# Performance work log

Hardware: AMD Instinct MI355X
Metric: run time of the kernel (lower is better)

The kernel has to match this reference:

```python
import jax, jax.numpy as jnp
import numpy as np

B, S, E, H, DH = 4, 2048, 1024, 16, 64
W_STD = 0.02  # init scale so softmax logits stay in a sane range


def setup_inputs() -> dict:
    key = jax.random.key(0)
    kx, kq, kk, kv, ko = jax.random.split(key, 5)
    x = jax.random.normal(kx, (B, S, E), dtype=jnp.float32)
    # torch nn.Linear weight layout is [out_features, in_features]; stacked over heads -> [H, DH, E]
    Wq = jax.random.normal(kq, (H, DH, E), dtype=jnp.float32) * W_STD
    Wk = jax.random.normal(kk, (H, DH, E), dtype=jnp.float32) * W_STD
    Wv = jax.random.normal(kv, (H, DH, E), dtype=jnp.float32) * W_STD
    Wo = jax.random.normal(ko, (E, E), dtype=jnp.float32) * W_STD
    return {"x": x, "Wq": Wq, "Wk": Wk, "Wv": Wv, "Wo": Wo}


def reference(x, Wq, Wk, Wv, Wo):
    Bx, Sx, Ex = x.shape
    head_dim = Wq.shape[1]
    scale = head_dim ** 0.5
    # Batched per-head projections (equivalent to the per-head Linear loop): y = x @ W.T
    q = jnp.einsum('bse,hde->bhsd', x, Wq)  # [B,H,S,DH]
    k = jnp.einsum('bse,hde->bhsd', x, Wk)
    v = jnp.einsum('bse,hde->bhsd', x, Wv)
    scores = jnp.einsum('bhsd,bhtd->bhst', q, k) / scale  # [B,H,S,S]
    causal = jnp.tril(jnp.ones((Sx, Sx), dtype=bool))
    scores = jnp.where(causal, scores, -jnp.inf)
    weights = jax.nn.softmax(scores, axis=-1)
    attn = jnp.einsum('bhst,bhtd->bshd', weights, v)  # [B,S,H,DH]
    concat = attn.reshape(Bx, Sx, Ex)  # head concat along feature dim
    return concat @ Wo.T
```

## Files before the change

### kernel.cpp

```cpp
#include <hip/hip_runtime.h>
#include <cstdint>
#include <cstddef>

typedef __bf16 bf16_t;
typedef __bf16 bf16x8 __attribute__((ext_vector_type(8)));
typedef float f32x4 __attribute__((ext_vector_type(4)));

#define MFMA16(a, b, c) __builtin_amdgcn_mfma_f32_16x16x32_bf16((a), (b), (c), 0, 0, 0)

__global__ __launch_bounds__(256) void cvt_f32_bf16(const float* __restrict__ src,
                                                    bf16_t* __restrict__ dst, int n4) {
  int stride = gridDim.x * blockDim.x;
  for (int i = blockIdx.x * blockDim.x + threadIdx.x; i < n4; i += stride) {
    float4 v = *(const float4*)(src + (size_t)i * 4);
    ushort4 o;
    o.x = __builtin_bit_cast(unsigned short, (bf16_t)v.x);
    o.y = __builtin_bit_cast(unsigned short, (bf16_t)v.y);
    o.z = __builtin_bit_cast(unsigned short, (bf16_t)v.z);
    o.w = __builtin_bit_cast(unsigned short, (bf16_t)v.w);
    *(ushort4*)(dst + (size_t)i * 4) = o;
  }
}

__global__ __launch_bounds__(256) void cvt3_f32_bf16(const float* __restrict__ s0,
                                                     const float* __restrict__ s1,
                                                     const float* __restrict__ s2,
                                                     bf16_t* __restrict__ dst, int n4) {
  const float* src = (blockIdx.y == 0) ? s0 : (blockIdx.y == 1) ? s1 : s2;
  bf16_t* d = dst + (size_t)blockIdx.y * n4 * 4;
  int stride = gridDim.x * blockDim.x;
  for (int i = blockIdx.x * blockDim.x + threadIdx.x; i < n4; i += stride) {
    float4 v = *(const float4*)(src + (size_t)i * 4);
    ushort4 o;
    o.x = __builtin_bit_cast(unsigned short, (bf16_t)v.x);
    o.y = __builtin_bit_cast(unsigned short, (bf16_t)v.y);
    o.z = __builtin_bit_cast(unsigned short, (bf16_t)v.z);
    o.w = __builtin_bit_cast(unsigned short, (bf16_t)v.w);
    *(ushort4*)(d + (size_t)i * 4) = o;
  }
}

__device__ __forceinline__ void gload_lds16(const bf16_t* g, bf16_t* lds) {
  __builtin_amdgcn_global_load_lds(
      (const __attribute__((address_space(1))) unsigned int*)g,
      (__attribute__((address_space(3))) unsigned int*)lds, 16, 0, 0);
}

__device__ __forceinline__ bf16x8 lds_frag(const bf16_t* tile, int row, int g) {
  int byte = row * 128 + ((g ^ (row & 7)) << 4);
  return *(const bf16x8*)((const char*)tile + byte);
}

__device__ __forceinline__ unsigned cvt_pk_bf16(float lo, float hi) {
  unsigned r;
  asm("v_cvt_pk_bf16_f32 %0, %1, %2" : "=v"(r) : "v"(lo), "v"(hi));
  return r;
}

template <int EPI>
__global__ __launch_bounds__(256)
void gemm_bt(const bf16_t* __restrict__ A, const bf16_t* __restrict__ Bm,
             bf16_t* __restrict__ Qo, bf16_t* __restrict__ Ko,
             bf16_t* __restrict__ Vto, float* __restrict__ Co) {
  const int K = 1024;
  const int NX = (EPI == 0) ? 24 : 8;
  __shared__ bf16_t As[128 * 64];
  __shared__ bf16_t Bs[128 * 64];
  const int wave = threadIdx.x >> 6, lane = threadIdx.x & 63;
  const int lm = lane & 15, lg = lane >> 4;
  const int wm = wave >> 1, wn = wave & 1;

  const int cpx = gridDim.x >> 3;
  const int swz = (blockIdx.x & 7) * cpx + (blockIdx.x >> 3);
  const int tm = (swz / NX) * 128, tn = (swz % NX) * 128;

  f32x4 zero = {0.f, 0.f, 0.f, 0.f};
  f32x4 acc[4][4];
#pragma unroll
  for (int i = 0; i < 4; ++i)
#pragma unroll
    for (int j = 0; j < 4; ++j) acc[i][j] = zero;

  const int srow = lane >> 3;
  const int gs = lane & 7;

  for (int k0 = 0; k0 < K; k0 += 64) {
#pragma unroll
    for (int c = 0; c < 4; ++c) {
      int cc = wave * 4 + c;
      int row = cc * 8 + srow;
      int gsrc = gs ^ (row & 7);
      gload_lds16(A + (size_t)(tm + row) * K + k0 + gsrc * 8, &As[cc * 512]);
      gload_lds16(Bm + (size_t)(tn + row) * K + k0 + gsrc * 8, &Bs[cc * 512]);
    }
    __syncthreads();
#pragma unroll
    for (int kk = 0; kk < 2; ++kk) {
      bf16x8 af[4], bfr[4];
#pragma unroll
      for (int i = 0; i < 4; ++i) af[i] = lds_frag(As, wm * 64 + i * 16 + lm, kk * 4 + lg);
#pragma unroll
      for (int i = 0; i < 4; ++i) bfr[i] = lds_frag(Bs, wn * 64 + i * 16 + lm, kk * 4 + lg);
#pragma unroll
      for (int mi = 0; mi < 4; ++mi)
#pragma unroll
        for (int ni = 0; ni < 4; ++ni)
          acc[mi][ni] = MFMA16(af[mi], bfr[ni], acc[mi][ni]);
    }
    __syncthreads();
  }

#pragma unroll
  for (int mi = 0; mi < 4; ++mi) {
#pragma unroll
    for (int ni = 0; ni < 4; ++ni) {
      const int m0 = tm + wm * 64 + mi * 16 + lg * 4;
      const int n = tn + wn * 64 + ni * 16 + lm;
      if (EPI == 0) {
        int which = n >> 10, rem = n & 1023;
        int hh = rem >> 6, d = rem & 63;
        int bb = m0 >> 11, s0 = m0 & 2047;
        size_t bh = (size_t)bb * 16 + hh;
        if (which == 2) {
          uint2 pw;
          pw.x = cvt_pk_bf16(acc[mi][ni][0], acc[mi][ni][1]);
          pw.y = cvt_pk_bf16(acc[mi][ni][2], acc[mi][ni][3]);
          *(uint2*)(Vto + (bh * 64 + d) * 2048 + s0) = pw;
        } else {
#pragma unroll
          for (int r = 0; r < 4; ++r) {
            float v = acc[mi][ni][r];
            if (which == 0)
              Qo[(bh * 2048 + s0 + r) * 64 + d] = (bf16_t)(v * 0.18033688011112042f);
            else
              Ko[(bh * 2048 + s0 + r) * 64 + d] = (bf16_t)v;
          }
        }
      } else {
#pragma unroll
        for (int r = 0; r < 4; ++r) Co[(size_t)(m0 + r) * 1024 + n] = acc[mi][ni][r];
      }
    }
  }
}

__device__ __forceinline__ void sm_step(const f32x4& s0, const f32x4& s1,
                                        float& l_run, bf16_t* P, int gbase,
                                        bool diag, int lm, int lg, int qrel) {
  float tv[2][4];
#pragma unroll
  for (int nt = 0; nt < 2; ++nt)
#pragma unroll
    for (int r = 0; r < 4; ++r) {
      float v = nt ? s1[r] : s0[r];
      if (diag && (nt * 16 + lg * 4 + r > qrel)) v = -3.0e38f;
      tv[nt][r] = v;
    }
#pragma unroll
  for (int nt = 0; nt < 2; ++nt) {
    float p0 = __builtin_amdgcn_exp2f(tv[nt][0]);
    float p1 = __builtin_amdgcn_exp2f(tv[nt][1]);
    float p2 = __builtin_amdgcn_exp2f(tv[nt][2]);
    float p3 = __builtin_amdgcn_exp2f(tv[nt][3]);
    l_run += (p0 + p1) + (p2 + p3);
    uint2 pw;
    pw.x = cvt_pk_bf16(p0, p1);
    pw.y = cvt_pk_bf16(p2, p3);
    int gr = (gbase + nt * 2 + (lg >> 1)) ^ (lm & 7);
    *(uint2*)((char*)P + lm * 128 + gr * 16 + (lg & 1) * 8) = pw;
  }
}

__device__ __forceinline__ void pv_step(const bf16_t* P, int gbase, const bf16x8 bv[4],
                                        f32x4* acc, int lm, int lg) {
  int gr = (gbase + lg) ^ (lm & 7);
  bf16x8 pf = *(const bf16x8*)((const char*)P + lm * 128 + gr * 16);
#pragma unroll
  for (int nd = 0; nd < 4; ++nd) acc[nd] = MFMA16(bv[nd], pf, acc[nd]);
}

__global__ __launch_bounds__(256, 4)
void attn_fwd(const bf16_t* __restrict__ Q, const bf16_t* __restrict__ K,
              const bf16_t* __restrict__ Vt, bf16_t* __restrict__ Aout) {
  const int S = 2048;
  const int i = blockIdx.x;
  const int bh = (i & 7) * 8 + ((i >> 3) & 7);
  const int p = i >> 6;
  const int hL = p, hH = 31 - p;
  const int b = bh >> 4, h = bh & 15;
  const int w = threadIdx.x >> 6, lane = threadIdx.x & 63;
  const int lm = lane & 15, lg = lane >> 4;
  const int qrowL = hL * 64 + w * 16;
  const int qrowH = hH * 64 + w * 16;
  const int qrel = ((w & 1) << 4) + lm;

  const bf16_t* Qb = Q + (size_t)bh * S * 64;
  const bf16_t* Kb = K + (size_t)bh * S * 64;
  const bf16_t* Vb = Vt + (size_t)bh * 64 * S;

  __shared__ bf16_t Plds[4][1024];
  __shared__ bf16_t Ksb[2][4096];
  __shared__ bf16_t Vsb[2][4096];
  bf16_t* P = Plds[w];

  bf16x8 aqL[2], aqH[2];
#pragma unroll
  for (int kk = 0; kk < 2; ++kk) {
    aqL[kk] = *(const bf16x8*)(Qb + (size_t)(qrowL + lm) * 64 + kk * 32 + lg * 8);
    aqH[kk] = *(const bf16x8*)(Qb + (size_t)(qrowH + lm) * 64 + kk * 32 + lg * 8);
  }

  float lL = 0.f, lH = 0.f;
  f32x4 zero = {0.f, 0.f, 0.f, 0.f};
  f32x4 accL[4], accH[4];
#pragma unroll
  for (int nd = 0; nd < 4; ++nd) { accL[nd] = zero; accH[nd] = zero; }

  const int sLend = hL * 2 + (w >> 1);
  const int sHend = hH * 2 + (w >> 1);

  auto stage = [&](int buf, int t) {
    const int kv0 = t * 64;
#pragma unroll
    for (int j = 0; j < 2; ++j) {
      int c = w * 2 + j;
      int r = c * 8 + (lane >> 3);
      int gs = (lane & 7) ^ (r & 7);
      gload_lds16(Kb + (size_t)(kv0 + r) * 64 + gs * 8, Ksb[buf] + c * 512);
      gload_lds16(Vb + (size_t)r * S + kv0 + gs * 8, Vsb[buf] + c * 512);
    }
  };

  stage(0, 0);
  for (int t = 0; t <= hH; ++t) {
    if (t < hH) {
      stage((t + 1) & 1, t + 1);
      asm volatile("s_waitcnt vmcnt(4)" ::: "memory");
    } else {
      asm volatile("s_waitcnt vmcnt(0)" ::: "memory");
    }
    __builtin_amdgcn_s_barrier();
    asm volatile("" ::: "memory");
    const bf16_t* Ks_ = Ksb[t & 1];
    const bf16_t* Vs_ = Vsb[t & 1];
#pragma unroll
    for (int s32 = 0; s32 < 2; ++s32) {
      const int step = t * 2 + s32;
      const bool actH = step <= sHend;
      const bool actL = step <= sLend;
      if (actH) {
        bf16x8 kf[2][2], bv[4];
#pragma unroll
        for (int nt = 0; nt < 2; ++nt)
#pragma unroll
          for (int kk = 0; kk < 2; ++kk)
            kf[nt][kk] = lds_frag(Ks_, s32 * 32 + nt * 16 + lm, kk * 4 + lg);
#pragma unroll
        for (int nd = 0; nd < 4; ++nd)
          bv[nd] = lds_frag(Vs_, nd * 16 + lm, s32 * 4 + lg);
        f32x4 sh0 = MFMA16(kf[0][0], aqH[0], zero);
        sh0 = MFMA16(kf[0][1], aqH[1], sh0);
        f32x4 sh1 = MFMA16(kf[1][0], aqH[0], zero);
        sh1 = MFMA16(kf[1][1], aqH[1], sh1);
        f32x4 sl0, sl1;
        if (actL) {
          sl0 = MFMA16(kf[0][0], aqL[0], zero);
          sl0 = MFMA16(kf[0][1], aqL[1], sl0);
          sl1 = MFMA16(kf[1][0], aqL[0], zero);
          sl1 = MFMA16(kf[1][1], aqL[1], sl1);
        }
        sm_step(sh0, sh1, lH, P, 4, step == sHend, lm, lg, qrel);
        if (actL) sm_step(sl0, sl1, lL, P, 0, step == sLend, lm, lg, qrel);
        asm volatile("s_waitcnt lgkmcnt(0)" ::: "memory");
        pv_step(P, 4, bv, accH, lm, lg);
        if (actL) pv_step(P, 0, bv, accL, lm, lg);
      }
    }
    asm volatile("" ::: "memory");
    __builtin_amdgcn_s_barrier();
    asm volatile("" ::: "memory");
  }

  float lsH = lH, lsL = lL;
  lsH += __shfl_xor(lsH, 16); lsH += __shfl_xor(lsH, 32);
  lsL += __shfl_xor(lsL, 16); lsL += __shfl_xor(lsL, 32);
  const float rlH = 1.f / lsH, rlL = 1.f / lsL;
#pragma unroll
  for (int nd = 0; nd < 4; ++nd) {
    uint2 oH, oL;
    oH.x = cvt_pk_bf16(accH[nd][0] * rlH, accH[nd][1] * rlH);
    oH.y = cvt_pk_bf16(accH[nd][2] * rlH, accH[nd][3] * rlH);
    oL.x = cvt_pk_bf16(accL[nd][0] * rlL, accL[nd][1] * rlL);
    oL.y = cvt_pk_bf16(accL[nd][2] * rlL, accL[nd][3] * rlL);
    size_t col = (size_t)(h * 64 + nd * 16 + lg * 4);
    *(uint2*)(Aout + ((size_t)(b * 2048 + qrowH + lm)) * 1024 + col) = oH;
    *(uint2*)(Aout + ((size_t)(b * 2048 + qrowL + lm)) * 1024 + col) = oL;
  }
}

extern "C" void kernel_launch(void* const* d_in, const int* in_sizes, int n_in,
                              void* d_out, int out_size, void* d_ws, size_t ws_size,
                              hipStream_t stream) {
  (void)in_sizes; (void)n_in; (void)out_size; (void)ws_size;
  const float* x  = (const float*)d_in[0];
  const float* Wq = (const float*)d_in[1];
  const float* Wk = (const float*)d_in[2];
  const float* Wv = (const float*)d_in[3];
  const float* Wo = (const float*)d_in[4];

  char* w = (char*)d_ws;
  bf16_t* xb    = (bf16_t*)(w);
  bf16_t* wb    = (bf16_t*)(w + 16777216);
  bf16_t* wob   = (bf16_t*)(w + 23068672);
  bf16_t* qb    = (bf16_t*)(w + 25165824);
  bf16_t* kb    = (bf16_t*)(w + 41943040);
  bf16_t* vtb   = (bf16_t*)(w + 58720256);
  bf16_t* attnb = (bf16_t*)(w + 75497472);

  cvt_f32_bf16<<<512, 256, 0, stream>>>(x, xb, 8388608 / 4);
  cvt3_f32_bf16<<<dim3(128, 3), 256, 0, stream>>>(Wq, Wk, Wv, wb, 1048576 / 4);
  cvt_f32_bf16<<<256, 256, 0, stream>>>(Wo, wob, 1048576 / 4);

  gemm_bt<0><<<dim3(1536), 256, 0, stream>>>(xb, wb, qb, kb, vtb, nullptr);
  attn_fwd<<<dim3(1024), 256, 0, stream>>>(qb, kb, vtb, attnb);
  gemm_bt<1><<<dim3(512), 256, 0, stream>>>(attnb, wob, nullptr, nullptr, nullptr,
                                            (float*)d_out);
}
```

Baseline: 168.5 us.

## Merge conversion kernels and share K/V tiles across two query pairs per block

Folds the three f32-to-bf16 conversion launches into one kernel with a 2D grid, which removes launch overhead. The attention kernel now runs 512 threads as two groups of four waves. Each group handles a different low/high query-tile pair of the same head, so one staged K/V tile in LDS serves twice as many queries and the number of blocks is halved. The cost is that the block loops to the longer pair's end, which brings some load imbalance and idle steps for the shorter group. Larger blocks with more LDS may also lower occupancy.

After: 164.2 us. -2.5%, faster.

```diff
diff --git a/kernel.cpp b/kernel.cpp
--- a/kernel.cpp
+++ b/kernel.cpp
@@ -8,8 +8,25 @@
 
 #define MFMA16(a, b, c) __builtin_amdgcn_mfma_f32_16x16x32_bf16((a), (b), (c), 0, 0, 0)
 
-__global__ __launch_bounds__(256) void cvt_f32_bf16(const float* __restrict__ src,
-                                                    bf16_t* __restrict__ dst, int n4) {
+__global__ __launch_bounds__(256) void cvt_all(const float* __restrict__ x,
+                                               const float* __restrict__ Wq,
+                                               const float* __restrict__ Wk,
+                                               const float* __restrict__ Wv,
+                                               const float* __restrict__ Wo,
+                                               bf16_t* __restrict__ xb,
+                                               bf16_t* __restrict__ wb,
+                                               bf16_t* __restrict__ wob) {
+  const int y = blockIdx.y;
+  const float* src;
+  bf16_t* dst;
+  if (y < 8) {
+    src = x + (size_t)y * 1048576;
+    dst = xb + (size_t)y * 1048576;
+  } else if (y == 8)  { src = Wq; dst = wb; }
+  else if (y == 9)    { src = Wk; dst = wb + 1048576; }
+  else if (y == 10)   { src = Wv; dst = wb + 2097152; }
+  else                { src = Wo; dst = wob; }
+  const int n4 = 262144;
   int stride = gridDim.x * blockDim.x;
   for (int i = blockIdx.x * blockDim.x + threadIdx.x; i < n4; i += stride) {
     float4 v = *(const float4*)(src + (size_t)i * 4);
@@ -19,24 +36,6 @@
     o.z = __builtin_bit_cast(unsigned short, (bf16_t)v.z);
     o.w = __builtin_bit_cast(unsigned short, (bf16_t)v.w);
     *(ushort4*)(dst + (size_t)i * 4) = o;
-  }
-}
-
-__global__ __launch_bounds__(256) void cvt3_f32_bf16(const float* __restrict__ s0,
-                                                     const float* __restrict__ s1,
-                                                     const float* __restrict__ s2,
-                                                     bf16_t* __restrict__ dst, int n4) {
-  const float* src = (blockIdx.y == 0) ? s0 : (blockIdx.y == 1) ? s1 : s2;
-  bf16_t* d = dst + (size_t)blockIdx.y * n4 * 4;
-  int stride = gridDim.x * blockDim.x;
-  for (int i = blockIdx.x * blockDim.x + threadIdx.x; i < n4; i += stride) {
-    float4 v = *(const float4*)(src + (size_t)i * 4);
-    ushort4 o;
-    o.x = __builtin_bit_cast(unsigned short, (bf16_t)v.x);
-    o.y = __builtin_bit_cast(unsigned short, (bf16_t)v.y);
-    o.z = __builtin_bit_cast(unsigned short, (bf16_t)v.z);
-    o.w = __builtin_bit_cast(unsigned short, (bf16_t)v.w);
-    *(ushort4*)(d + (size_t)i * 4) = o;
   }
 }
 
@@ -179,26 +178,29 @@
   for (int nd = 0; nd < 4; ++nd) acc[nd] = MFMA16(bv[nd], pf, acc[nd]);
 }
 
-__global__ __launch_bounds__(256, 4)
+__global__ __launch_bounds__(512, 8)
 void attn_fwd(const bf16_t* __restrict__ Q, const bf16_t* __restrict__ K,
               const bf16_t* __restrict__ Vt, bf16_t* __restrict__ Aout) {
   const int S = 2048;
   const int i = blockIdx.x;
   const int bh = (i & 7) * 8 + ((i >> 3) & 7);
-  const int p = i >> 6;
-  const int hL = p, hH = 31 - p;
+  const int j = i >> 6;
   const int b = bh >> 4, h = bh & 15;
   const int w = threadIdx.x >> 6, lane = threadIdx.x & 63;
   const int lm = lane & 15, lg = lane >> 4;
-  const int qrowL = hL * 64 + w * 16;
-  const int qrowH = hH * 64 + w * 16;
-  const int qrel = ((w & 1) << 4) + lm;
+  const int g = w >> 2;
+  const int wg = w & 3;
+  const int p = j + 8 * g;
+  const int hL = p, hH = 31 - p;
+  const int qrowL = hL * 64 + wg * 16;
+  const int qrowH = hH * 64 + wg * 16;
+  const int qrel = ((wg & 1) << 4) + lm;
 
   const bf16_t* Qb = Q + (size_t)bh * S * 64;
   const bf16_t* Kb = K + (size_t)bh * S * 64;
   const bf16_t* Vb = Vt + (size_t)bh * 64 * S;
 
-  __shared__ bf16_t Plds[4][1024];
+  __shared__ bf16_t Plds[8][1024];
   __shared__ bf16_t Ksb[2][4096];
   __shared__ bf16_t Vsb[2][4096];
   bf16_t* P = Plds[w];
@@ -216,26 +218,24 @@
 #pragma unroll
   for (int nd = 0; nd < 4; ++nd) { accL[nd] = zero; accH[nd] = zero; }
 
-  const int sLend = hL * 2 + (w >> 1);
-  const int sHend = hH * 2 + (w >> 1);
+  const int sLend = hL * 2 + (wg >> 1);
+  const int sHend = hH * 2 + (wg >> 1);
+  const int tmax = 31 - j;
 
   auto stage = [&](int buf, int t) {
     const int kv0 = t * 64;
-#pragma unroll
-    for (int j = 0; j < 2; ++j) {
-      int c = w * 2 + j;
-      int r = c * 8 + (lane >> 3);
-      int gs = (lane & 7) ^ (r & 7);
-      gload_lds16(Kb + (size_t)(kv0 + r) * 64 + gs * 8, Ksb[buf] + c * 512);
-      gload_lds16(Vb + (size_t)r * S + kv0 + gs * 8, Vsb[buf] + c * 512);
-    }
+    int c = w;
+    int r = c * 8 + (lane >> 3);
+    int gs = (lane & 7) ^ (r & 7);
+    gload_lds16(Kb + (size_t)(kv0 + r) * 64 + gs * 8, Ksb[buf] + c * 512);
+    gload_lds16(Vb + (size_t)r * S + kv0 + gs * 8, Vsb[buf] + c * 512);
   };
 
   stage(0, 0);
-  for (int t = 0; t <= hH; ++t) {
-    if (t < hH) {
+  for (int t = 0; t <= tmax; ++t) {
+    if (t < tmax) {
       stage((t + 1) & 1, t + 1);
-      asm volatile("s_waitcnt vmcnt(4)" ::: "memory");
+      asm volatile("s_waitcnt vmcnt(2)" ::: "memory");
     } else {
       asm volatile("s_waitcnt vmcnt(0)" ::: "memory");
     }
@@ -317,12 +317,10 @@
   bf16_t* vtb   = (bf16_t*)(w + 58720256);
   bf16_t* attnb = (bf16_t*)(w + 75497472);
 
-  cvt_f32_bf16<<<512, 256, 0, stream>>>(x, xb, 8388608 / 4);
-  cvt3_f32_bf16<<<dim3(128, 3), 256, 0, stream>>>(Wq, Wk, Wv, wb, 1048576 / 4);
-  cvt_f32_bf16<<<256, 256, 0, stream>>>(Wo, wob, 1048576 / 4);
+  cvt_all<<<dim3(128, 12), 256, 0, stream>>>(x, Wq, Wk, Wv, Wo, xb, wb, wob);
 
   gemm_bt<0><<<dim3(1536), 256, 0, stream>>>(xb, wb, qb, kb, vtb, nullptr);
-  attn_fwd<<<dim3(1024), 256, 0, stream>>>(qb, kb, vtb, attnb);
+  attn_fwd<<<dim3(512), 512, 0, stream>>>(qb, kb, vtb, attnb);
   gemm_bt<1><<<dim3(512), 256, 0, stream>>>(attnb, wob, nullptr, nullptr, nullptr,
                                             (float*)d_out);
 }
```
